# Optimization experiments

Hardware: AMD Instinct MI355X
Metric: run time of the kernel (lower is better)

The kernel has to match this reference:

```python
import jax, jax.numpy as jnp
import numpy as np
from jax import lax

KS = 3
N = KS * KS  # 9 sampling locations per output pixel


def conv2d(x, w, b, pad, dil=1):
    out = lax.conv_general_dilated(
        x, w, window_strides=(1, 1), padding=((pad, pad), (pad, pad)),
        rhs_dilation=(dil, dil), dimension_numbers=('NCHW', 'OIHW', 'NCHW'))
    return out + b[None, :, None, None]


def deform_conv(x, p_w, p_b, dw, db):
    # Pure deform-conv-v2 semantics: offsets from p_conv, bilinear gather on
    # zero-padded input, then 3x3 contraction over the 9 gathered samples.
    B, C, H, W = x.shape
    offset = conv2d(x, p_w, p_b, 1)                       # (B, 2N, H, W)
    xp = jnp.pad(x, ((0, 0), (0, 0), (1, 1), (1, 1)))     # zero pad by 1
    Hp, Wp = H + 2, W + 2
    rr = jnp.arange(-(KS // 2), KS // 2 + 1)
    pi, pj = jnp.meshgrid(rr, rr, indexing='ij')
    p_n = jnp.concatenate([pi.reshape(-1), pj.reshape(-1)]).astype(x.dtype)   # (2N,)
    gi, gj = jnp.meshgrid(jnp.arange(1, H + 1), jnp.arange(1, W + 1), indexing='ij')
    p0 = jnp.concatenate([jnp.broadcast_to(gi, (N, H, W)),
                          jnp.broadcast_to(gj, (N, H, W))], 0).astype(x.dtype)  # (2N,H,W)
    p = p0[None] + p_n[None, :, None, None] + offset      # (B, 2N, H, W)
    p = jnp.transpose(p, (0, 2, 3, 1))                    # (B, H, W, 2N)
    py, px = p[..., :N], p[..., N:]
    fy, fx = jnp.floor(py), jnp.floor(px)
    lt_y = jnp.clip(fy, 0, Hp - 1); lt_x = jnp.clip(fx, 0, Wp - 1)
    rb_y = jnp.clip(fy + 1, 0, Hp - 1); rb_x = jnp.clip(fx + 1, 0, Wp - 1)
    pyc = jnp.clip(py, 0, Hp - 1); pxc = jnp.clip(px, 0, Wp - 1)
    g_lt = (1 + (lt_y - pyc)) * (1 + (lt_x - pxc))
    g_rb = (1 - (rb_y - pyc)) * (1 - (rb_x - pxc))
    g_lb = (1 + (lt_y - pyc)) * (1 - (rb_x - pxc))
    g_rt = (1 - (rb_y - pyc)) * (1 + (lt_x - pxc))
    xf = xp.reshape(B, C, Hp * Wp)

    def gather(qy, qx):
        idx = (qy.astype(jnp.int32) * Wp + qx.astype(jnp.int32)).reshape(B, -1)
        g = jax.vmap(lambda xb, ib: jnp.take(xb, ib, axis=1))(xf, idx)
        return g.reshape(B, C, H, W, N)

    x_lt = gather(lt_y, lt_x); x_rb = gather(rb_y, rb_x)
    x_lb = gather(lt_y, rb_x); x_rt = gather(rb_y, lt_x)
    samples = (g_lt[:, None] * x_lt + g_rb[:, None] * x_rb
               + g_lb[:, None] * x_lb + g_rt[:, None] * x_rt)  # (B,C,H,W,N)
    out = jnp.einsum('bchwn,ocn->bohw', samples, dw.reshape(dw.shape[0], C, N))
    return out + db[None, :, None, None]


def reference(x, w1, b1, w2, b2, w3, b3, w4, b4, p_w, p_b, dw, db, cw, cb):
    branches = [(w1, b1, 1, 1.0), (w2, b2, 3, 3.0), (w3, b3, 5, 5.0), (w4, b4, 7, 7.0)]
    feats = [deform_conv(conv2d(x, w, b, d, d) * s, p_w, p_b, dw, db)
             for (w, b, d, s) in branches]
    combined = jnp.concatenate(feats, axis=1)             # (B, 4*Cout, H, W)
    return jax.nn.relu(conv2d(combined, cw, cb, 0))


def setup_inputs() -> dict:
    B, Cin, Cout, H, W = 4, 128, 64, 128, 128
    key = jax.random.key(0)
    ks = jax.random.split(key, 16)
    sc3 = 1.0 / np.sqrt(Cin * 9)      # fan-in scale for 3x3 convs
    sc1 = 1.0 / np.sqrt(4 * Cout)     # fan-in scale for 1x1 fuse conv
    scd = 1.0 / np.sqrt(Cout * 9)     # deform main conv
    inp = {'x': jax.random.normal(ks[0], (B, Cin, H, W), jnp.float32)}
    for i in range(4):
        inp[f'w{i+1}'] = jax.random.normal(ks[1 + i], (Cout, Cin, 3, 3), jnp.float32) * sc3
        inp[f'b{i+1}'] = jax.random.normal(ks[5 + i], (Cout,), jnp.float32) * 0.01
    inp['p_w'] = jax.random.normal(ks[9], (2 * N, Cout, 3, 3), jnp.float32) * 0.01
    inp['p_b'] = jax.random.normal(ks[10], (2 * N,), jnp.float32) * 0.01
    inp['dw'] = jax.random.normal(ks[11], (Cout, Cout, 3, 3), jnp.float32) * scd
    inp['db'] = jax.random.normal(ks[12], (Cout,), jnp.float32) * 0.01
    inp['cw'] = jax.random.normal(ks[13], (Cout, 4 * Cout, 1, 1), jnp.float32) * sc1
    inp['cb'] = jax.random.normal(ks[14], (Cout,), jnp.float32) * 0.01
    return inp
```

## Files before the change

### kernel.cpp

```cpp
#include <hip/hip_runtime.h>
#include <hip/hip_fp16.h>

#define H 128
#define W 128
#define CIN 128
#define COUT 64
#define HW (H*W)
#define XW 130
#define FSL (XW*XW*64)
#define XTD 144

typedef __half f16;
typedef __attribute__((ext_vector_type(8)))  _Float16 h16x8;
typedef __attribute__((ext_vector_type(16))) float f32x16;

__device__ __forceinline__ float b2f(f16 v){ return __half2float(v); }
__device__ __forceinline__ f16  f2b(float v){ return __float2half_rn(v); }
__device__ __forceinline__ unsigned pack2(float a, float b){
    unsigned short ua = __builtin_bit_cast(unsigned short, f2b(a));
    unsigned short ub = __builtin_bit_cast(unsigned short, f2b(b));
    return (unsigned)ua | ((unsigned)ub << 16);
}
__device__ __forceinline__ unsigned short b16u(float v){
    return __builtin_bit_cast(unsigned short, f2b(v));
}
__device__ __forceinline__ __half2 uh2(unsigned u){
    return __builtin_bit_cast(__half2, u);
}
__device__ __forceinline__ unsigned h2u(__half2 v){
    return __builtin_bit_cast(unsigned, v);
}
__device__ __forceinline__ unsigned bcasth2(float v){
    __half h = __float2half_rn(v);
    return h2u(__halves2half2(h, h));
}

__global__ __launch_bounds__(256) void k_prep(
    const float* __restrict__ w1, const float* __restrict__ w2,
    const float* __restrict__ w3, const float* __restrict__ w4,
    const float* __restrict__ dw, const float* __restrict__ cw,
    const float* __restrict__ pw,
    uint4* __restrict__ xt4, unsigned* __restrict__ wbt,
    unsigned* __restrict__ dwb2, unsigned* __restrict__ cwb2,
    unsigned* __restrict__ pwb)
{
    int bid = blockIdx.x;
    int t = threadIdx.x;
    if (bid < 1024){
        const int n4 = (4*XTD*XTD*64)/4;
        for (int i = bid*256 + t; i < n4; i += 1024*256)
            xt4[i] = make_uint4(0,0,0,0);
    } else if (bid < 1600){
        int tid = (bid-1024)*256 + t;
        int cpl = tid & 7;
        int oc  = (tid >> 3) & 63;
        int tap = (tid >> 9) % 9;
        int cg  = (tid / 4608) & 7;
        int d   = tid / 36864;
        const float* wt = (d==0)?w1:(d==1)?w2:(d==2)?w3:w4;
        int c = cg*8 + cpl;
        wbt[tid] = pack2(wt[((size_t)oc*CIN + 2*c  )*9 + tap],
                         wt[((size_t)oc*CIN + 2*c+1)*9 + tap]);
    } else if (bid < 1672){
        int i = (bid-1600)*256 + t;
        int n = i>>11, oc = (i>>5)&63, cp = i&31;
        dwb2[i] = pack2(dw[((size_t)oc*64 + 2*cp  )*9 + n],
                        dw[((size_t)oc*64 + 2*cp+1)*9 + n]);
    } else if (bid < 1704){
        int i = (bid-1672)*256 + t;
        int oc = i>>7, cp = i&127;
        cwb2[i] = pack2(cw[(size_t)oc*256 + 2*cp], cw[(size_t)oc*256 + 2*cp+1]);
    } else {
        int i = (bid-1704)*256 + t;
        int cl = i & 3, oc = (i>>2)&31, hf = (i>>7)&1, cq = (i>>8)&3, tap = i>>10;
        int c = cq*16 + hf*8 + cl*2;
        unsigned v = 0u;
        if (oc < 18)
            v = pack2(pw[((size_t)oc*64 + c  )*9 + tap],
                      pw[((size_t)oc*64 + c+1)*9 + tap]);
        pwb[i] = v;
    }
}

__global__ __launch_bounds__(256) void k_xprep(
    const float* __restrict__ x, unsigned* __restrict__ xt)
{
    int y = blockIdx.x, b = blockIdx.y;
    int t = threadIdx.x;
    __shared__ float xsm[64*131];
    for (int ci0 = 0; ci0 < 128; ci0 += 64){
        for (int i=0;i<32;i++){
            int idx = t + 256*i;
            int col = idx & 127, ci = idx >> 7;
            xsm[ci*131 + col] = x[(((size_t)b*CIN + ci0+ci)*H + y)*W + col];
        }
        __syncthreads();
        for (int i=0;i<16;i++){
            int idx = t + 256*i;
            int cpg = idx & 31, col = idx >> 5;
            int cgg = (ci0 >> 4) + (cpg >> 3);
            int cpl = cpg & 7;
            unsigned u = pack2(xsm[(2*cpg)*131 + col], xsm[(2*cpg+1)*131 + col]);
            xt[((((size_t)b*8 + cgg)*XTD + y+8)*XTD + col+8)*8 + cpl] = u;
        }
        __syncthreads();
    }
}

__global__ __launch_bounds__(256,2) void k_branch_mfma(
    const unsigned* __restrict__ xt, const unsigned* __restrict__ wbt,
    const float* __restrict__ b1, const float* __restrict__ b2,
    const float* __restrict__ b3, const float* __restrict__ b4,
    f16* __restrict__ feats2)
{
    int bid = blockIdx.x;
    int xcd = bid & 7;
    int j   = bid >> 3;
    int zb  = xcd + 8*(j & 1);
    int hp  = j >> 1;
    int d = zb >> 2, b = zb & 3;
    int dil = 2*d + 1;
    int h0 = hp*2;
    const float* bs = (d==0)?b1:(d==1)?b2:(d==2)?b3:b4;
    const float scale = (float)dil;

    __shared__ unsigned smem[10368 + 6912];
    unsigned* As = smem;
    unsigned* Bs = smem + 10368;
    const unsigned short* As16 = (const unsigned short*)As;
    const unsigned short* Bs16 = (const unsigned short*)Bs;

    int t = threadIdx.x;
    int lane = t & 63;
    int w = t >> 6;
    int l31 = lane & 31;
    int half = lane >> 5;

    f16* fb = feats2 + (size_t)zb*FSL;
    if (t < 32){
        int yy = h0 + 1 + (t>>4);
        int side = (t>>3)&1;
        int q = t & 7;
        uint4 z = make_uint4(0,0,0,0);
        *(uint4*)((unsigned short*)fb + ((size_t)yy*XW + side*129)*64 + q*8) = z;
    }
    if (hp == 0){
        uint4 z = make_uint4(0,0,0,0);
        for (int i=t; i<2080; i+=256){
            int row = i / 1040;
            int r = i % 1040;
            int xx = r >> 3, q = r & 7;
            *(uint4*)((unsigned short*)fb + ((size_t)(row*129)*XW + xx)*64 + q*8) = z;
        }
    }

    f32x16 acc[2][2];
    #pragma unroll
    for (int i=0;i<2;i++)
      #pragma unroll
      for (int jj=0;jj<2;jj++)
        #pragma unroll
        for (int e=0;e<16;e++) acc[i][jj][e] = 0.f;

    const unsigned* xtb_b = xt + (size_t)b*8*XTD*XTD*8;
    int r = w >> 1;
    int pxb = (w & 1) * 64;

    for (int cg=0; cg<8; cg++){
        const unsigned* xs_cg = xtb_b + (size_t)cg*XTD*XTD*8;
        #pragma unroll
        for (int i=0;i<7;i++){
            int idx4 = t + 256*i;
            if (idx4 < 1728){
                int cp4 = idx4 & 1;
                int s   = (idx4 >> 1) % 144;
                int row6= idx4 / 288;
                int ky = row6 >> 1, rr = row6 & 1;
                int yy = h0 + rr + (ky-1)*dil + 8;
                uint4 v = *(const uint4*)(xs_cg + ((size_t)yy*XTD + (s + 8 - dil))*8 + cp4*4);
                *(uint4*)&As[(row6*144 + s)*12 + cp4*4] = v;
            }
        }
        const unsigned* wb_cg = wbt + ((size_t)d*8 + cg)*4608;
        #pragma unroll
        for (int i=0;i<5;i++){
            int idx4 = t + 256*i;
            if (idx4 < 1152){
                int cp4 = idx4 & 1;
                int oc  = (idx4 >> 1) & 63;
                int tap = idx4 >> 7;
                uint4 v = *(const uint4*)(wb_cg + ((size_t)tap*64 + oc)*8 + cp4*4);
                *(uint4*)&Bs[(tap*64 + oc)*12 + cp4*4] = v;
            }
        }
        __syncthreads();
        #pragma unroll
        for (int tap=0; tap<9; tap++){
            int ky = tap/3, kx = tap%3;
            int rowb = (ky*2 + r)*144;
            h16x8 a0 = *(const h16x8*)(As16 + (rowb + pxb      + l31 + kx*dil)*24 + half*8);
            h16x8 a1 = *(const h16x8*)(As16 + (rowb + pxb + 32 + l31 + kx*dil)*24 + half*8);
            h16x8 bb0 = *(const h16x8*)(Bs16 + (tap*64      + l31)*24 + half*8);
            h16x8 bb1 = *(const h16x8*)(Bs16 + (tap*64 + 32 + l31)*24 + half*8);
            acc[0][0] = __builtin_amdgcn_mfma_f32_32x32x16_f16(a0, bb0, acc[0][0], 0,0,0);
            acc[0][1] = __builtin_amdgcn_mfma_f32_32x32x16_f16(a0, bb1, acc[0][1], 0,0,0);
            acc[1][0] = __builtin_amdgcn_mfma_f32_32x32x16_f16(a1, bb0, acc[1][0], 0,0,0);
            acc[1][1] = __builtin_amdgcn_mfma_f32_32x32x16_f16(a1, bb1, acc[1][1], 0,0,0);
        }
        __syncthreads();
    }

    unsigned short* ep = (unsigned short*)smem;
    float bias0 = bs[l31], bias1 = bs[32 + l31];
    #pragma unroll
    for (int i=0;i<2;i++){
      #pragma unroll
      for (int jj=0;jj<2;jj++){
        int oc = jj*32 + l31;
        float bj = jj ? bias1 : bias0;
        #pragma unroll
        for (int rg=0; rg<4; rg++){
            int m0 = 64*w + 32*i + 8*rg + 4*half;
            #pragma unroll
            for (int e=0;e<4;e++)
                ep[(m0+e)*64 + oc] = b16u((acc[i][jj][4*rg+e] + bj)*scale);
        }
      }
    }
    __syncthreads();
    {
        int row = t >> 7, pxm = t & 127;
        unsigned short* drow = (unsigned short*)fb + ((size_t)(h0+1+row)*XW + pxm + 1)*64;
        const unsigned short* srow = ep + t*64;
        #pragma unroll
        for (int q=0;q<8;q++)
            *(uint4*)(drow + q*8) = *(const uint4*)(srow + q*8);
    }
}

__global__ __launch_bounds__(256,2) void k_offset_mfma(
    const f16* __restrict__ feats2,
    const unsigned* __restrict__ pwb,
    const float* __restrict__ pb,
    f16* __restrict__ offs)
{
    int bid = blockIdx.x;
    int xcd  = bid & 7;
    int h    = (bid >> 3) & 127;
    int pass = bid >> 10;
    int zb   = xcd + 8*pass;

    int t = threadIdx.x;
    int lane = t & 63, w = t >> 6;
    int l31 = lane & 31, half = lane >> 5;

    __shared__ unsigned short xs[3*132*68];

    const unsigned short* fin = (const unsigned short*)(feats2 + (size_t)zb*FSL);
    for (int i=t; i<3120; i+=256){
        int row = i / 1040;
        int r   = i % 1040;
        int col = r >> 3, q = r & 7;
        uint4 v = *(const uint4*)(fin + ((size_t)(h+row)*XW + col)*64 + q*8);
        *(uint4*)&xs[(row*132 + col)*68 + q*8] = v;
    }
    __syncthreads();

    f32x16 acc;
    #pragma unroll
    for (int e=0;e<16;e++) acc[e] = 0.f;

    int pxw = 32*w + l31;
    #pragma unroll
    for (int tap=0; tap<9; tap++){
        int ky = tap/3, kx = tap%3;
        const unsigned short* arow = &xs[(ky*132 + pxw + kx)*68 + half*8];
        const unsigned* brow = pwb + (((size_t)tap*4)*2 + half)*128 + l31*4;
        #pragma unroll
        for (int cq=0; cq<4; cq++){
            h16x8 a  = *(const h16x8*)(arow + cq*16);
            h16x8 b0 = *(const h16x8*)(brow + cq*256);
            acc = __builtin_amdgcn_mfma_f32_32x32x16_f16(a, b0, acc, 0,0,0);
        }
    }
    __syncthreads();

    unsigned short* ep = (unsigned short*)xs;
    if (l31 < 18){
        float bias = pb[l31];
        #pragma unroll
        for (int rg=0; rg<4; rg++){
            int m0 = 32*w + 4*half + 8*rg;
            #pragma unroll
            for (int e=0;e<4;e++)
                ep[l31*132 + m0+e] = b16u(acc[4*rg+e] + bias);
        }
    }
    __syncthreads();
    unsigned short* obase = (unsigned short*)(offs + (size_t)zb*18*HW) ;
    for (int i=t; i<288; i+=256){
        int oc = i >> 4, sg = i & 15;
        *(uint4*)(obase + (size_t)oc*HW + h*W + sg*8) = *(const uint4*)(ep + oc*132 + sg*8);
    }
}

__global__ __launch_bounds__(256,4) void k_deform_mfma(
    const f16* __restrict__ feats2,
    const f16* __restrict__ offs,
    const unsigned* __restrict__ dwb2,
    const float* __restrict__ db,
    f16* __restrict__ dout2)
{
    int bid = blockIdx.x;
    int xcd  = bid & 7;
    int h    = (bid >> 3) & 127;
    int pass = bid >> 10;
    int zb   = xcd + 8*pass;

    int t = threadIdx.x;
    int lane = t & 63, w = t >> 6;
    int l31 = lane & 31, half = lane >> 5;
    int pxg = t >> 3;
    int cq  = t & 7;
    int sub_w = cq >> 1;
    int hf8   = cq & 1;

    #define AROW 516
    __shared__ unsigned smem_d[8*AROW + 2304 + 1024];
    unsigned* Asu = smem_d;
    unsigned* Bsu = smem_d + 8*AROW;
    unsigned* Cd  = smem_d + 8*AROW + 2304;

    const f16* obase = offs + (size_t)zb*18*HW + h*W;
    const unsigned short* fbase = (const unsigned short*)(feats2 + (size_t)zb*FSL);

    f32x16 acc0, acc1;
    #pragma unroll
    for (int e=0;e<16;e++){ acc0[e]=0.f; acc1[e]=0.f; }

    for (int n=0; n<9; n++){
        const uint4* dsrc = (const uint4*)(dwb2 + n*2048);
        #pragma unroll
        for (int i=0;i<2;i++){
            int j = t + 256*i;
            int idx4 = j*4;
            int oc = idx4 >> 5, cp = idx4 & 31;
            *(uint4*)&Bsu[oc*36 + cp] = dsrc[j];
        }
        if (t < 128){
            float offy = b2f(obase[n*HW + t]);
            float offx = b2f(obase[(n+9)*HW + t]);
            float py  = (float)(h + n/3) + offy;
            float pxf = (float)(t + n%3) + offx;
            float fy = floorf(py), fx = floorf(pxf);
            float lty = fminf(fmaxf(fy,     0.f),129.f);
            float ltx = fminf(fmaxf(fx,     0.f),129.f);
            float rby = fminf(fmaxf(fy+1.f, 0.f),129.f);
            float rbx = fminf(fmaxf(fx+1.f, 0.f),129.f);
            float pyc = fminf(fmaxf(py,     0.f),129.f);
            float pxc = fminf(fmaxf(pxf,    0.f),129.f);
            float ay = 1.f + (lty-pyc), by = 1.f - (rby-pyc);
            float ax = 1.f + (ltx-pxc), bx = 1.f - (rbx-pxc);
            unsigned* cp = &Cd[t*8];
            cp[0] = bcasth2(ay*ax);
            cp[1] = bcasth2(ay*bx);
            cp[2] = bcasth2(by*ax);
            cp[3] = bcasth2(by*bx);
            cp[4] = (unsigned)(((int)lty*XW + (int)ltx)*64);
            cp[5] = (unsigned)(((int)rbx - (int)ltx)*64);
            cp[6] = (unsigned)(((int)rby - (int)lty)*XW*64);
        }
        __syncthreads();
        #pragma unroll
        for (int s=0; s<4; s++){
            int px = s*32 + pxg;
            const unsigned* cp = &Cd[px*8];
            uint4 c0 = *(const uint4*)cp;
            uint4 c1 = *(const uint4*)(cp + 4);
            __half2 wlt = uh2(c0.x);
            __half2 wlb = uh2(c0.y);
            __half2 wrt = uh2(c0.z);
            __half2 wrb = uh2(c0.w);
            int base = (int)c1.x;
            int dxo  = (int)c1.y;
            int dyo  = (int)c1.z;

            const unsigned short* fc = fbase + base + cq*8;
            unsigned LT[4], LB[4], RT[4], RB[4];
            *(uint4*)LT = *(const uint4*)(fc);
            *(uint4*)LB = *(const uint4*)(fc+dxo);
            *(uint4*)RT = *(const uint4*)(fc+dyo);
            *(uint4*)RB = *(const uint4*)(fc+dyo+dxo);
            unsigned pk[4];
            #pragma unroll
            for (int jq=0;jq<4;jq++){
                __half2 r = __hmul2(wlt, uh2(LT[jq]));
                r = __hfma2(wlb, uh2(LB[jq]), r);
                r = __hfma2(wrt, uh2(RT[jq]), r);
                r = __hfma2(wrb, uh2(RB[jq]), r);
                pk[jq] = h2u(r);
            }
            uint4 av; av.x=pk[0]; av.y=pk[1]; av.z=pk[2]; av.w=pk[3];
            *(uint4*)&Asu[(sub_w*2 + hf8)*AROW + px*4] = av;
        }
        __syncthreads();
        const unsigned short* As16 = (const unsigned short*)Asu;
        const unsigned short* Bs16 = (const unsigned short*)Bsu;
        #pragma unroll
        for (int s=0;s<4;s++){
            h16x8 a  = *(const h16x8*)(As16 + (s*2+half)*(AROW*2) + (32*w + l31)*8);
            h16x8 b0 = *(const h16x8*)(Bs16 + (l31*36 + s*8 + half*4)*2);
            h16x8 b1 = *(const h16x8*)(Bs16 + ((32+l31)*36 + s*8 + half*4)*2);
            acc0 = __builtin_amdgcn_mfma_f32_32x32x16_f16(a, b0, acc0, 0,0,0);
            acc1 = __builtin_amdgcn_mfma_f32_32x32x16_f16(a, b1, acc1, 0,0,0);
        }
        __syncthreads();
    }

    unsigned short* ep = (unsigned short*)smem_d;
    #pragma unroll
    for (int nt=0; nt<2; nt++){
        int oc = nt*32 + l31;
        float bias = db[oc];
        const f32x16& A = nt ? acc1 : acc0;
        #pragma unroll
        for (int rg=0; rg<4; rg++){
            int m0 = 32*w + 4*half + 8*rg;
            #pragma unroll
            for (int e=0;e<4;e++)
                ep[(m0+e)*64 + oc] = b16u(A[4*rg+e] + bias);
        }
    }
    __syncthreads();
    uint4* dst = (uint4*)((unsigned short*)dout2 + ((size_t)zb*128 + h)*(128*64));
    #pragma unroll
    for (int i=0;i<4;i++)
        dst[t + 256*i] = ((const uint4*)ep)[t + 256*i];
    #undef AROW
}

__global__ __launch_bounds__(256,2) void k_combine_mfma(
    const f16* __restrict__ dout2,
    const unsigned* __restrict__ cwb2,
    const float* __restrict__ cb,
    float* __restrict__ out)
{
    int h = blockIdx.x, b = blockIdx.y;
    int t = threadIdx.x;
    int px = t & 127, hf = t >> 7;
    int lane = t & 63, w = t >> 6, l31 = lane & 31, half = lane >> 5;

    __shared__ unsigned Bsu[64*132];
    __shared__ unsigned Asu2[1024];

    for (int i=t; i<8192; i+=256){
        int oc = i>>7, cp = i&127;
        Bsu[oc*132 + cp] = cwb2[i];
    }
    f32x16 acc0, acc1;
    #pragma unroll
    for (int e=0;e<16;e++){ acc0[e]=0.f; acc1[e]=0.f; }

    const unsigned short* dbase0 = (const unsigned short*)dout2;
    size_t rowsel = ((size_t)b*128 + h)*128 + px;
    uint4 v = *(const uint4*)(dbase0 + rowsel*64 + hf*8);
    for (int kc=0; kc<16; kc++){
        *(uint4*)&Asu2[(hf*128+px)*4] = v;
        __syncthreads();
        if (kc < 15){
            int kn = kc+1;
            int d = kn>>2, c16 = kn&3;
            v = *(const uint4*)(dbase0 + ((size_t)d*4*128*128*64 + rowsel*64) + c16*16 + hf*8);
        }
        const unsigned short* As16 = (const unsigned short*)Asu2;
        const unsigned short* Bs16 = (const unsigned short*)Bsu;
        h16x8 a  = *(const h16x8*)(As16 + (half*128 + 32*w + l31)*8);
        h16x8 b0 = *(const h16x8*)(Bs16 + (l31*132 + kc*8 + half*4)*2);
        h16x8 b1 = *(const h16x8*)(Bs16 + ((32+l31)*132 + kc*8 + half*4)*2);
        acc0 = __builtin_amdgcn_mfma_f32_32x32x16_f16(a, b0, acc0, 0,0,0);
        acc1 = __builtin_amdgcn_mfma_f32_32x32x16_f16(a, b1, acc1, 0,0,0);
        __syncthreads();
    }
    float* ep = (float*)Bsu;
    #pragma unroll
    for (int nt=0; nt<2; nt++){
        int oc = nt*32 + l31;
        float bias = cb[oc];
        const f32x16& A = nt ? acc1 : acc0;
        #pragma unroll
        for (int rg=0; rg<4; rg++){
            int m0 = 32*w + 4*half + 8*rg;
            #pragma unroll
            for (int e=0;e<4;e++)
                ep[oc*132 + m0+e] = fmaxf(A[4*rg+e] + bias, 0.f);
        }
    }
    __syncthreads();
    for (int i=t; i<2048; i+=256){
        int oc = i>>5, sg = i&31;
        *(uint4*)&out[(((size_t)b*64+oc)*128 + h)*128 + sg*4] = *(const uint4*)&ep[oc*132 + sg*4];
    }
}

extern "C" void kernel_launch(void* const* d_in, const int* in_sizes, int n_in,
                              void* d_out, int out_size, void* d_ws, size_t ws_size,
                              hipStream_t stream) {
    const float* x  = (const float*)d_in[0];
    const float* w1 = (const float*)d_in[1];
    const float* b1 = (const float*)d_in[2];
    const float* w2 = (const float*)d_in[3];
    const float* b2 = (const float*)d_in[4];
    const float* w3 = (const float*)d_in[5];
    const float* b3 = (const float*)d_in[6];
    const float* w4 = (const float*)d_in[7];
    const float* b4 = (const float*)d_in[8];
    const float* pw = (const float*)d_in[9];
    const float* pb = (const float*)d_in[10];
    const float* dw = (const float*)d_in[11];
    const float* db = (const float*)d_in[12];
    const float* cw = (const float*)d_in[13];
    const float* cb = (const float*)d_in[14];
    float* out = (float*)d_out;

    f16* feats2 = (f16*)d_ws;
    f16* offs   = feats2 + (size_t)16*FSL;
    f16* region2 = offs + (size_t)16*18*HW;
    f16* dout2  = region2;
    unsigned* xt  = (unsigned*)region2;
    unsigned* wbt = xt + (size_t)4*8*XTD*XTD*8;
    unsigned* dwb2 = (unsigned*)(dout2 + (size_t)16*128*128*64);
    unsigned* cwb2 = dwb2 + 18432;
    unsigned* pwb  = cwb2 + 8192;

    k_prep        <<<dim3(1740),    256, 0, stream>>>(w1,w2,w3,w4, dw, cw, pw,
                                                      (uint4*)xt, wbt, dwb2, cwb2, pwb);
    k_xprep       <<<dim3(128,4),   256, 0, stream>>>(x, xt);
    k_branch_mfma <<<dim3(1024),    256, 0, stream>>>(xt, wbt, b1,b2,b3,b4, feats2);
    k_offset_mfma <<<dim3(2048),    256, 0, stream>>>(feats2, pwb, pb, offs);
    k_deform_mfma <<<dim3(2048),    256, 0, stream>>>(feats2, offs, dwb2, db, dout2);
    k_combine_mfma<<<dim3(128,4),   256, 0, stream>>>(dout2, cwb2, cb, out);
}
```

Measured before the change: 320.3 us.

## Use direct global-to-LDS loads with compact half-split layout in branch conv

Replaces register-staged global loads plus LDS stores in the dilated branch conv with global_load_lds 16-byte direct transfers, and reorganizes the LDS tiles into a half-split layout with no padding. This shrinks shared memory per block and raises the launch-bounds occupancy hint from 2 to 3 blocks per CU. The unpadded layout may bring LDS bank conflicts on the MFMA operand reads, and with no double buffering the loads still serialize with compute.

```diff
diff --git a/kernel.cpp b/kernel.cpp
--- a/kernel.cpp
+++ b/kernel.cpp
@@ -33,6 +33,11 @@
 __device__ __forceinline__ unsigned bcasth2(float v){
     __half h = __float2half_rn(v);
     return h2u(__halves2half2(h, h));
+}
+__device__ __forceinline__ void gld16(const void* g, void* l){
+    __builtin_amdgcn_global_load_lds(
+        (const __attribute__((address_space(1))) void*)g,
+        (__attribute__((address_space(3))) void*)l, 16, 0, 0);
 }
 
 __global__ __launch_bounds__(256) void k_prep(
@@ -107,7 +112,7 @@
     }
 }
 
-__global__ __launch_bounds__(256,2) void k_branch_mfma(
+__global__ __launch_bounds__(256,3) void k_branch_mfma(
     const unsigned* __restrict__ xt, const unsigned* __restrict__ wbt,
     const float* __restrict__ b1, const float* __restrict__ b2,
     const float* __restrict__ b3, const float* __restrict__ b4,
@@ -124,9 +129,9 @@
     const float* bs = (d==0)?b1:(d==1)?b2:(d==2)?b3:b4;
     const float scale = (float)dil;
 
-    __shared__ unsigned smem[10368 + 6912];
+    __shared__ unsigned smem[6912 + 4608];
     unsigned* As = smem;
-    unsigned* Bs = smem + 10368;
+    unsigned* Bs = smem + 6912;
     const unsigned short* As16 = (const unsigned short*)As;
     const unsigned short* Bs16 = (const unsigned short*)Bs;
 
@@ -172,13 +177,14 @@
         for (int i=0;i<7;i++){
             int idx4 = t + 256*i;
             if (idx4 < 1728){
-                int cp4 = idx4 & 1;
-                int s   = (idx4 >> 1) % 144;
-                int row6= idx4 / 288;
+                int row6 = idx4 / 288;
+                int rem  = idx4 - row6*288;
+                int hf   = rem / 144;
+                int s    = rem - hf*144;
                 int ky = row6 >> 1, rr = row6 & 1;
                 int yy = h0 + rr + (ky-1)*dil + 8;
-                uint4 v = *(const uint4*)(xs_cg + ((size_t)yy*XTD + (s + 8 - dil))*8 + cp4*4);
-                *(uint4*)&As[(row6*144 + s)*12 + cp4*4] = v;
+                gld16(xs_cg + ((size_t)yy*XTD + (s + 8 - dil))*8 + hf*4,
+                      &As[idx4*4]);
             }
         }
         const unsigned* wb_cg = wbt + ((size_t)d*8 + cg)*4608;
@@ -186,22 +192,23 @@
         for (int i=0;i<5;i++){
             int idx4 = t + 256*i;
             if (idx4 < 1152){
-                int cp4 = idx4 & 1;
-                int oc  = (idx4 >> 1) & 63;
                 int tap = idx4 >> 7;
-                uint4 v = *(const uint4*)(wb_cg + ((size_t)tap*64 + oc)*8 + cp4*4);
-                *(uint4*)&Bs[(tap*64 + oc)*12 + cp4*4] = v;
+                int hf  = (idx4 >> 6) & 1;
+                int oc  = idx4 & 63;
+                gld16(wb_cg + ((size_t)tap*64 + oc)*8 + hf*4,
+                      &Bs[idx4*4]);
             }
         }
         __syncthreads();
         #pragma unroll
         for (int tap=0; tap<9; tap++){
             int ky = tap/3, kx = tap%3;
-            int rowb = (ky*2 + r)*144;
-            h16x8 a0 = *(const h16x8*)(As16 + (rowb + pxb      + l31 + kx*dil)*24 + half*8);
-            h16x8 a1 = *(const h16x8*)(As16 + (rowb + pxb + 32 + l31 + kx*dil)*24 + half*8);
-            h16x8 bb0 = *(const h16x8*)(Bs16 + (tap*64      + l31)*24 + half*8);
-            h16x8 bb1 = *(const h16x8*)(Bs16 + (tap*64 + 32 + l31)*24 + half*8);
+            int arow = ((ky*2 + r)*2 + half)*144;
+            int brow = (tap*2 + half)*64;
+            h16x8 a0  = *(const h16x8*)(As16 + (arow + pxb      + l31 + kx*dil)*8);
+            h16x8 a1  = *(const h16x8*)(As16 + (arow + pxb + 32 + l31 + kx*dil)*8);
+            h16x8 bb0 = *(const h16x8*)(Bs16 + (brow      + l31)*8);
+            h16x8 bb1 = *(const h16x8*)(Bs16 + (brow + 32 + l31)*8);
             acc[0][0] = __builtin_amdgcn_mfma_f32_32x32x16_f16(a0, bb0, acc[0][0], 0,0,0);
             acc[0][1] = __builtin_amdgcn_mfma_f32_32x32x16_f16(a0, bb1, acc[0][1], 0,0,0);
             acc[1][0] = __builtin_amdgcn_mfma_f32_32x32x16_f16(a1, bb0, acc[1][0], 0,0,0);
```

New measurement: 299.0 us. -6.6%, faster.
